# Kernel tuning notes

Hardware: AMD Instinct MI355X
Metric: run time of the kernel (lower is better)

Reference implementation:

```python
import jax, jax.numpy as jnp
import numpy as np


def quantize_uniform(x, n_bits, clip):
    # clamp to [-clip, clip], round to 2^(1-n_bits)*clip grid, cap at clip*(1-b)
    b = 2.0 ** (1 - n_bits)
    xc = jnp.clip(x, -clip, clip)
    return clip * jnp.minimum(b * jnp.round(xc / (b * clip)), 1.0 - b)


def quantize_act(x, n_bits, clip):
    # clip to [0, clip], round to 2^-n_bits grid, cap at 1 - 2^-n_bits
    s = 2.0 ** n_bits
    xc = jnp.clip(x, 0.0, clip)
    return jnp.minimum(jnp.round(xc * s) / s, 1.0 - 1.0 / s)


def qconv(x, w, b, pad):
    # fake-quantized conv: weights/bias quant(8,1), input quant(8,4), output quant(8,8)
    wq = quantize_uniform(w, 8, 1.0)
    bq = quantize_uniform(b, 8, 1.0)
    xq = quantize_uniform(x, 8, 4.0)
    y = jax.lax.conv_general_dilated(
        xq, wq, window_strides=(1, 1), padding=[(pad, pad), (pad, pad)],
        dimension_numbers=('NCHW', 'OIHW', 'NCHW'))
    y = y + bq[None, :, None, None]
    return quantize_uniform(y, 8, 8.0)


def setup_inputs() -> dict:
    key = jax.random.key(0)
    ks = jax.random.split(key, 7)
    N, Cin, H, W = 32, 128, 56, 56
    Sq, E1, E3 = 32, 128, 128
    x = jax.random.normal(ks[0], (N, Cin, H, W), dtype=jnp.float32)
    w_sq = jax.random.normal(ks[1], (Sq, Cin, 1, 1), dtype=jnp.float32) * 0.05
    b_sq = jax.random.normal(ks[2], (Sq,), dtype=jnp.float32) * 0.05
    w_e1 = jax.random.normal(ks[3], (E1, Sq, 1, 1), dtype=jnp.float32) * 0.05
    b_e1 = jax.random.normal(ks[4], (E1,), dtype=jnp.float32) * 0.05
    w_e3 = jax.random.normal(ks[5], (E3, Sq, 3, 3), dtype=jnp.float32) * 0.05
    b_e3 = jax.random.normal(ks[6], (E3,), dtype=jnp.float32) * 0.05
    return {'x': x, 'w_sq': w_sq, 'b_sq': b_sq, 'w_e1': w_e1, 'b_e1': b_e1,
            'w_e3': w_e3, 'b_e3': b_e3}


def reference(x, w_sq, b_sq, w_e1, b_e1, w_e3, b_e3):
    h = jax.nn.relu(qconv(x, w_sq, b_sq, pad=0))
    h = quantize_act(h, 13, 4.0)
    y1 = jax.nn.relu(qconv(h, w_e1, b_e1, pad=0))
    y3 = jax.nn.relu(qconv(h, w_e3, b_e3, pad=1))
    return jnp.concatenate([y1, y3], axis=1)
```

## Files before the change

kernel.cpp:

```cpp
#include <hip/hip_runtime.h>
#include <stdint.h>

typedef __bf16 bf16x8 __attribute__((ext_vector_type(8)));
typedef float  f32x4  __attribute__((ext_vector_type(4)));

#define HW   3136
#define WID  56
#define CIN  128
#define SQ   32
#define NPIX 100352

#define OFF_WSQ 0
#define OFF_BSQ 4096
#define OFF_BE  4128
#define WE1F_BYTES_OFF 17536
#define WE3F_BYTES_OFF 25728
#define HQ_BYTES_OFF   99456

__device__ __forceinline__ float quant_w8(float x){
  float xc = fminf(fmaxf(x,-1.f),1.f);
  return fminf(rintf(xc*128.f)*0.0078125f, 0.9921875f);
}
__device__ __forceinline__ ushort wq_int_bf16(float x){
  float xc = fminf(fmaxf(x,-1.f),1.f);
  float n = fminf(rintf(xc*128.f), 127.f);
  return (ushort)(__float_as_uint(n)>>16);
}
__device__ __forceinline__ uint pack2(uint k0, uint k1){
  return (__float_as_uint((float)k0)>>16) | (__float_as_uint((float)k1)&0xffff0000u);
}

__global__ void prep_kernel(const float* __restrict__ wsq, const float* __restrict__ bsq,
                            const float* __restrict__ we1, const float* __restrict__ be1,
                            const float* __restrict__ we3, const float* __restrict__ be3,
                            float* __restrict__ ws){
  int tid = blockIdx.x*blockDim.x+threadIdx.x;
  int nth = gridDim.x*blockDim.x;
  ushort* we1f = (ushort*)((char*)ws + WE1F_BYTES_OFF);
  ushort* we3f = (ushort*)((char*)ws + WE3F_BYTES_OFF);
  for (int i=tid;i<SQ*CIN;i+=nth){ int co=i>>7, ci=i&127; ws[OFF_WSQ+ci*SQ+co]=quant_w8(wsq[i]); }
  for (int i=tid;i<SQ;i+=nth) ws[OFF_BSQ+i]=quant_w8(bsq[i]);
  for (int i=tid;i<256;i+=nth) ws[OFF_BE+i] = (i<128)? quant_w8(be1[i]) : quant_w8(be3[i-128]);
  for (int i=tid;i<4096;i+=nth){
    int mf=i>>9, l=(i>>3)&63, j=i&7;
    int co=mf*16+(l&15), ci=(l>>4)*8+j;
    we1f[i] = wq_int_bf16(we1[co*SQ+ci]);
  }
  for (int i=tid;i<36864;i+=nth){
    int mf=i/4608, r=i-mf*4608, t=r>>9, l=(r>>3)&63, j=r&7;
    int co=mf*16+(l&15), ci=(l>>4)*8+j;
    we3f[i] = wq_int_bf16(we3[(co*SQ+ci)*9+t]);
  }
}

__global__ __launch_bounds__(256) void squeeze_kernel(const float* __restrict__ x,
    const float* __restrict__ ws, uint8_t* __restrict__ hq){
  int pix = blockIdx.x*256+threadIdx.x;
  int half = blockIdx.y;
  int n = pix/HW, rem = pix-n*HW;
  const float* xp = x + (size_t)n*CIN*HW + rem;
  const float* wq = ws + OFF_WSQ + half*16;
  float acc[16];
  #pragma unroll
  for (int j=0;j<16;++j) acc[j]=0.f;
  #pragma unroll 8
  for (int ci=0;ci<CIN;++ci){
    float xv = xp[(size_t)ci*HW];
    xv = fminf(fmaxf(xv,-4.f),4.f);
    xv = fminf(rintf(xv*32.f)*0.03125f, 3.96875f);
    const float* wrow = wq + ci*SQ;
    #pragma unroll
    for (int j=0;j<16;++j) acc[j]=fmaf(xv,wrow[j],acc[j]);
  }
  uint32_t pk[4];
  #pragma unroll
  for (int q=0;q<4;++q){
    uint32_t p=0;
    #pragma unroll
    for (int b=0;b<4;++b){
      int j=q*4+b;
      float y = acc[j] + ws[OFF_BSQ+half*16+j];
      y = fminf(fmaxf(y,-8.f),8.f);
      y = fminf(rintf(y*16.f)*0.0625f, 7.9375f);
      y = fmaxf(y,0.f);
      y = fminf(y,4.f);
      y = fminf(y,0.9998779296875f);
      uint32_t m = (uint32_t)(int)rintf(y*32.f);
      p |= m<<(8*b);
    }
    pk[q]=p;
  }
  *(uint4*)(hq + (size_t)pix*32 + half*16) = make_uint4(pk[0],pk[1],pk[2],pk[3]);
}

__global__ __launch_bounds__(256) void expand_kernel(const uint8_t* __restrict__ hq,
    const float* __restrict__ ws, float* __restrict__ out){
  __shared__ uint4 lds4[232*4];
  int br = blockIdx.x;
  int n  = blockIdx.y;
  int tid = threadIdx.x;

  if (tid < 232){
    int r = tid/58, c = tid - r*58;
    int gy = br*2 + r - 1, gx = c - 1;
    uint4 v0, v1;
    if ((unsigned)gy < 56u && (unsigned)gx < 56u){
      const uint4* src = (const uint4*)(hq + ((size_t)(n*HW + gy*WID + gx))*32);
      v0 = src[0]; v1 = src[1];
    } else { v0 = make_uint4(0,0,0,0); v1 = v0; }
    uint w8[8] = {v0.x,v0.y,v0.z,v0.w,v1.x,v1.y,v1.z,v1.w};
    #pragma unroll
    for (int cc=0;cc<4;++cc){
      uint a = w8[cc*2], b = w8[cc*2+1];
      uint4 o;
      o.x = pack2(a&255u, (a>>8)&255u);
      o.y = pack2((a>>16)&255u, a>>24);
      o.z = pack2(b&255u, (b>>8)&255u);
      o.w = pack2((b>>16)&255u, b>>24);
      lds4[tid*4 + (cc ^ ((tid>>1)&3))] = o;
    }
  }
  __syncthreads();

  int lane = tid&63, wid = tid>>6;
  int colg = lane&15, kg = lane>>4;
  int baseh[7];
  #pragma unroll
  for (int nf=0;nf<7;++nf){
    int p = nf*16 + colg;
    int row = p/56, xx = p - row*56;
    baseh[nf] = (row+1)*58 + xx + 1;
  }
  float bias_v[4][4];
  #pragma unroll
  for (int mi=0;mi<4;++mi)
    #pragma unroll
    for (int r=0;r<4;++r)
      bias_v[mi][r] = ws[OFF_BE + (wid+mi*4)*16 + kg*4 + r];

  f32x4 acc[4][7];
  #pragma unroll
  for (int mi=0;mi<4;++mi)
    #pragma unroll
    for (int nf=0;nf<7;++nf)
      acc[mi][nf] = (f32x4){0.f,0.f,0.f,0.f};

  const bf16x8* we1f = (const bf16x8*)((const char*)ws + WE1F_BYTES_OFF);
  const bf16x8* we3f = (const bf16x8*)((const char*)ws + WE3F_BYTES_OFF);
  const bf16x8* lbase = (const bf16x8*)lds4;

  #pragma unroll
  for (int t=0;t<9;++t){
    int off = (t/3 - 1)*58 + (t%3 - 1);
    bf16x8 B[7];
    #pragma unroll
    for (int nf=0;nf<7;++nf){
      int ph = baseh[nf] + off;
      int idx = ph*4 + (kg ^ ((ph>>1)&3));
      B[nf] = lbase[idx];
    }
    bf16x8 A2 = we3f[(wid*9+t)*64 + lane];
    bf16x8 A3 = we3f[((wid+4)*9+t)*64 + lane];
    #pragma unroll
    for (int nf=0;nf<7;++nf){
      acc[2][nf] = __builtin_amdgcn_mfma_f32_16x16x32_bf16(A2, B[nf], acc[2][nf], 0,0,0);
      acc[3][nf] = __builtin_amdgcn_mfma_f32_16x16x32_bf16(A3, B[nf], acc[3][nf], 0,0,0);
    }
    if (t==4){
      bf16x8 A0 = we1f[wid*64 + lane];
      bf16x8 A1 = we1f[(wid+4)*64 + lane];
      #pragma unroll
      for (int nf=0;nf<7;++nf){
        acc[0][nf] = __builtin_amdgcn_mfma_f32_16x16x32_bf16(A0, B[nf], acc[0][nf], 0,0,0);
        acc[1][nf] = __builtin_amdgcn_mfma_f32_16x16x32_bf16(A1, B[nf], acc[1][nf], 0,0,0);
      }
    }
  }

  #pragma unroll
  for (int mi=0;mi<4;++mi){
    int co = (wid+mi*4)*16 + kg*4;
    #pragma unroll
    for (int nf=0;nf<7;++nf){
      int opix = br*112 + nf*16 + colg;
      float* op = out + (size_t)(n*256+co)*HW + opix;
      #pragma unroll
      for (int r=0;r<4;++r){
        float y = fmaf(acc[mi][nf][r], 0.000244140625f, bias_v[mi][r]);
        y = fminf(fmaxf(y,-8.f),8.f);
        y = fminf(rintf(y*16.f)*0.0625f, 7.9375f);
        y = fmaxf(y,0.f);
        op[(size_t)r*HW] = y;
      }
    }
  }
}

extern "C" void kernel_launch(void* const* d_in, const int* in_sizes, int n_in,
                              void* d_out, int out_size, void* d_ws, size_t ws_size,
                              hipStream_t stream){
  const float* x   = (const float*)d_in[0];
  const float* wsq = (const float*)d_in[1];
  const float* bsq = (const float*)d_in[2];
  const float* we1 = (const float*)d_in[3];
  const float* be1 = (const float*)d_in[4];
  const float* we3 = (const float*)d_in[5];
  const float* be3 = (const float*)d_in[6];
  float* out = (float*)d_out;
  float* ws  = (float*)d_ws;
  uint8_t* hq = (uint8_t*)d_ws + HQ_BYTES_OFF;

  hipLaunchKernelGGL(prep_kernel, dim3(64), dim3(256), 0, stream,
                     wsq, bsq, we1, be1, we3, be3, ws);
  hipLaunchKernelGGL(squeeze_kernel, dim3(NPIX/256, 2), dim3(256), 0, stream, x, ws, hq);
  hipLaunchKernelGGL(expand_kernel, dim3(28, 32), dim3(256), 0, stream, hq, ws, out);
}
```

Before: 54.14 us.

## Move squeeze conv to bf16 MFMA and vectorize expand output stores

The squeeze 1x1 conv now runs on MFMA instead of scalar FMA loops. Weights and inputs are quantized to exact integer-valued bf16 fragments, so each x element is read once rather than twice across the two channel halves. In the expand kernel the MFMA operands are swapped so each lane holds four consecutive pixels of one output channel. That lets the epilogue issue 16-byte nontemporal vector stores instead of scattered scalar stores. The cost is a changed workspace layout and per-lane strided scalar loads of x, which may coalesce less well.

```diff
diff --git a/kernel.cpp b/kernel.cpp
--- a/kernel.cpp
+++ b/kernel.cpp
@@ -10,12 +10,12 @@
 #define SQ   32
 #define NPIX 100352
 
-#define OFF_WSQ 0
-#define OFF_BSQ 4096
-#define OFF_BE  4128
-#define WE1F_BYTES_OFF 17536
-#define WE3F_BYTES_OFF 25728
-#define HQ_BYTES_OFF   99456
+#define OFF_BSQ 0
+#define OFF_BE  32
+#define WSQF_BYTES_OFF 1152
+#define WE1F_BYTES_OFF 9344
+#define WE3F_BYTES_OFF 17536
+#define HQ_BYTES_OFF   91264
 
 __device__ __forceinline__ float quant_w8(float x){
   float xc = fminf(fmaxf(x,-1.f),1.f);
@@ -36,11 +36,17 @@
                             float* __restrict__ ws){
   int tid = blockIdx.x*blockDim.x+threadIdx.x;
   int nth = gridDim.x*blockDim.x;
+  ushort* wsqf = (ushort*)((char*)ws + WSQF_BYTES_OFF);
   ushort* we1f = (ushort*)((char*)ws + WE1F_BYTES_OFF);
   ushort* we3f = (ushort*)((char*)ws + WE3F_BYTES_OFF);
-  for (int i=tid;i<SQ*CIN;i+=nth){ int co=i>>7, ci=i&127; ws[OFF_WSQ+ci*SQ+co]=quant_w8(wsq[i]); }
   for (int i=tid;i<SQ;i+=nth) ws[OFF_BSQ+i]=quant_w8(bsq[i]);
   for (int i=tid;i<256;i+=nth) ws[OFF_BE+i] = (i<128)? quant_w8(be1[i]) : quant_w8(be3[i-128]);
+  for (int i=tid;i<4096;i+=nth){
+    int mfkc=i>>9, l=(i>>3)&63, j=i&7;
+    int mf=mfkc>>2, kc=mfkc&3;
+    int co=mf*16+(l&15), ci=kc*32+(l>>4)*8+j;
+    wsqf[i] = wq_int_bf16(wsq[co*CIN+ci]);
+  }
   for (int i=tid;i<4096;i+=nth){
     int mf=i>>9, l=(i>>3)&63, j=i&7;
     int co=mf*16+(l&15), ci=(l>>4)*8+j;
@@ -55,42 +61,68 @@
 
 __global__ __launch_bounds__(256) void squeeze_kernel(const float* __restrict__ x,
     const float* __restrict__ ws, uint8_t* __restrict__ hq){
-  int pix = blockIdx.x*256+threadIdx.x;
-  int half = blockIdx.y;
-  int n = pix/HW, rem = pix-n*HW;
-  const float* xp = x + (size_t)n*CIN*HW + rem;
-  const float* wq = ws + OFF_WSQ + half*16;
-  float acc[16];
-  #pragma unroll
-  for (int j=0;j<16;++j) acc[j]=0.f;
-  #pragma unroll 8
-  for (int ci=0;ci<CIN;++ci){
-    float xv = xp[(size_t)ci*HW];
-    xv = fminf(fmaxf(xv,-4.f),4.f);
-    xv = fminf(rintf(xv*32.f)*0.03125f, 3.96875f);
-    const float* wrow = wq + ci*SQ;
-    #pragma unroll
-    for (int j=0;j<16;++j) acc[j]=fmaf(xv,wrow[j],acc[j]);
-  }
-  uint32_t pk[4];
-  #pragma unroll
-  for (int q=0;q<4;++q){
-    uint32_t p=0;
-    #pragma unroll
-    for (int b=0;b<4;++b){
-      int j=q*4+b;
-      float y = acc[j] + ws[OFF_BSQ+half*16+j];
-      y = fminf(fmaxf(y,-8.f),8.f);
-      y = fminf(rintf(y*16.f)*0.0625f, 7.9375f);
-      y = fmaxf(y,0.f);
-      y = fminf(y,4.f);
-      y = fminf(y,0.9998779296875f);
-      uint32_t m = (uint32_t)(int)rintf(y*32.f);
-      p |= m<<(8*b);
-    }
-    pk[q]=p;
-  }
-  *(uint4*)(hq + (size_t)pix*32 + half*16) = make_uint4(pk[0],pk[1],pk[2],pk[3]);
+  int tid = threadIdx.x, wid = tid>>6, lane = tid&63;
+  int colg = lane&15, kg = lane>>4;
+  const bf16x8* wsqf = (const bf16x8*)((const char*)ws + WSQF_BYTES_OFF);
+  bf16x8 W[8];
+  #pragma unroll
+  for (int q=0;q<8;++q) W[q] = wsqf[q*64 + lane];
+  float bias[2][4];
+  #pragma unroll
+  for (int mf=0;mf<2;++mf)
+    #pragma unroll
+    for (int r=0;r<4;++r) bias[mf][r] = ws[OFF_BSQ + mf*16 + kg*4 + r];
+
+  int blk0 = (blockIdx.x*4 + wid)*4;
+  for (int b=0;b<4;++b){
+    int pixbase = (blk0+b)*16;
+    int n = pixbase/HW;
+    int rem = pixbase - n*HW + colg;
+    const float* xp = x + (size_t)n*CIN*HW + rem;
+    bf16x8 Bf[4];
+    #pragma unroll
+    for (int kc=0;kc<4;++kc){
+      uint w0=0,w1=0,w2=0,w3=0;
+      #pragma unroll
+      for (int j=0;j<8;++j){
+        float xv = xp[(size_t)(kc*32 + kg*8 + j)*HW];
+        xv = fminf(fmaxf(xv,-4.f),4.f);
+        float m = fminf(rintf(xv*32.f), 127.f);
+        uint u = __float_as_uint(m)>>16;
+        if (j<2)      w0 |= u<<(16*(j&1));
+        else if (j<4) w1 |= u<<(16*(j&1));
+        else if (j<6) w2 |= u<<(16*(j&1));
+        else          w3 |= u<<(16*(j&1));
+      }
+      union { uint u[4]; bf16x8 v; } cv;
+      cv.u[0]=w0; cv.u[1]=w1; cv.u[2]=w2; cv.u[3]=w3;
+      Bf[kc] = cv.v;
+    }
+    f32x4 acc0 = (f32x4){0.f,0.f,0.f,0.f};
+    f32x4 acc1 = (f32x4){0.f,0.f,0.f,0.f};
+    #pragma unroll
+    for (int kc=0;kc<4;++kc){
+      acc0 = __builtin_amdgcn_mfma_f32_16x16x32_bf16(W[kc],   Bf[kc], acc0, 0,0,0);
+      acc1 = __builtin_amdgcn_mfma_f32_16x16x32_bf16(W[4+kc], Bf[kc], acc1, 0,0,0);
+    }
+    #pragma unroll
+    for (int mf=0;mf<2;++mf){
+      f32x4 a = mf ? acc1 : acc0;
+      uint p=0;
+      #pragma unroll
+      for (int r=0;r<4;++r){
+        float y = fmaf(a[r], 0.000244140625f, bias[mf][r]);
+        y = fminf(fmaxf(y,-8.f),8.f);
+        y = fminf(rintf(y*16.f)*0.0625f, 7.9375f);
+        y = fmaxf(y,0.f);
+        y = fminf(y,4.f);
+        y = fminf(y,0.9998779296875f);
+        uint m = (uint)(int)rintf(y*32.f);
+        p |= m<<(8*r);
+      }
+      *(uint*)(hq + (size_t)(pixbase+colg)*32 + mf*16 + kg*4) = p;
+    }
+  }
 }
 
 __global__ __launch_bounds__(256) void expand_kernel(const uint8_t* __restrict__ hq,
@@ -131,12 +163,6 @@
     int row = p/56, xx = p - row*56;
     baseh[nf] = (row+1)*58 + xx + 1;
   }
-  float bias_v[4][4];
-  #pragma unroll
-  for (int mi=0;mi<4;++mi)
-    #pragma unroll
-    for (int r=0;r<4;++r)
-      bias_v[mi][r] = ws[OFF_BE + (wid+mi*4)*16 + kg*4 + r];
 
   f32x4 acc[4][7];
   #pragma unroll
@@ -163,35 +189,38 @@
     bf16x8 A3 = we3f[((wid+4)*9+t)*64 + lane];
     #pragma unroll
     for (int nf=0;nf<7;++nf){
-      acc[2][nf] = __builtin_amdgcn_mfma_f32_16x16x32_bf16(A2, B[nf], acc[2][nf], 0,0,0);
-      acc[3][nf] = __builtin_amdgcn_mfma_f32_16x16x32_bf16(A3, B[nf], acc[3][nf], 0,0,0);
+      acc[2][nf] = __builtin_amdgcn_mfma_f32_16x16x32_bf16(B[nf], A2, acc[2][nf], 0,0,0);
+      acc[3][nf] = __builtin_amdgcn_mfma_f32_16x16x32_bf16(B[nf], A3, acc[3][nf], 0,0,0);
     }
     if (t==4){
       bf16x8 A0 = we1f[wid*64 + lane];
       bf16x8 A1 = we1f[(wid+4)*64 + lane];
       #pragma unroll
       for (int nf=0;nf<7;++nf){
-        acc[0][nf] = __builtin_amdgcn_mfma_f32_16x16x32_bf16(A0, B[nf], acc[0][nf], 0,0,0);
-        acc[1][nf] = __builtin_amdgcn_mfma_f32_16x16x32_bf16(A1, B[nf], acc[1][nf], 0,0,0);
+        acc[0][nf] = __builtin_amdgcn_mfma_f32_16x16x32_bf16(B[nf], A0, acc[0][nf], 0,0,0);
+        acc[1][nf] = __builtin_amdgcn_mfma_f32_16x16x32_bf16(B[nf], A1, acc[1][nf], 0,0,0);
       }
     }
   }
 
   #pragma unroll
   for (int mi=0;mi<4;++mi){
-    int co = (wid+mi*4)*16 + kg*4;
+    int co = (wid+mi*4)*16 + colg;
+    float bias = ws[OFF_BE + co];
+    float* opb = out + (size_t)(n*256+co)*HW + br*112 + kg*4;
     #pragma unroll
     for (int nf=0;nf<7;++nf){
-      int opix = br*112 + nf*16 + colg;
-      float* op = out + (size_t)(n*256+co)*HW + opix;
+      f32x4 a = acc[mi][nf];
+      f32x4 yv;
       #pragma unroll
       for (int r=0;r<4;++r){
-        float y = fmaf(acc[mi][nf][r], 0.000244140625f, bias_v[mi][r]);
+        float y = fmaf(a[r], 0.000244140625f, bias);
         y = fminf(fmaxf(y,-8.f),8.f);
         y = fminf(rintf(y*16.f)*0.0625f, 7.9375f);
         y = fmaxf(y,0.f);
-        op[(size_t)r*HW] = y;
-      }
+        yv[r] = y;
+      }
+      __builtin_nontemporal_store(yv, (f32x4*)(opb + nf*16));
     }
   }
 }
@@ -212,6 +241,6 @@
 
   hipLaunchKernelGGL(prep_kernel, dim3(64), dim3(256), 0, stream,
                      wsq, bsq, we1, be1, we3, be3, ws);
-  hipLaunchKernelGGL(squeeze_kernel, dim3(NPIX/256, 2), dim3(256), 0, stream, x, ws, hq);
+  hipLaunchKernelGGL(squeeze_kernel, dim3(NPIX/256), dim3(256), 0, stream, x, ws, hq);
   hipLaunchKernelGGL(expand_kernel, dim3(28, 32), dim3(256), 0, stream, hq, ws, out);
 }
```

Result: slower. 57.11 us (+5.5%).
